# Kernel optimization log

Hardware: AMD Instinct MI355X
Metric: run time of the kernel (lower is better)

## Reference

```python
import jax, jax.numpy as jnp
import numpy as np


def setup_inputs() -> dict:
    key = jax.random.key(0)
    M, D = 131072, 16
    x = jax.random.normal(key, (M, D), dtype=jnp.float32)
    return {"x": x, "n_segs": 64, "k": 16}


def reference(x, n_segs, k):
    """Segmented kNN graph: for each point set (segment), find each point's k
    nearest neighbors (L2) within its own segment and emit edges knn -> node,
    with node ids globally offset by the segment start (sum_{p<i} |V_p| + j).

    Returns
    -------
    dists : [M, k] float32  squared L2 distance to each of the k neighbors
    src   : [M, k] int32    global node ids of the k predecessors of each node
    dst   : [M]    int32    global node ids (dst of the k edges in each row)
    """
    M, D = x.shape
    S = M // n_segs  # points per segment (equal-sized segments)
    xs = x.reshape(n_segs, S, D)                              # [N, S, D]
    sq = jnp.sum(xs * xs, axis=-1)                            # [N, S]
    # squared pairwise distances per segment: ||a||^2 + ||b||^2 - 2 a.b
    dist = sq[:, :, None] + sq[:, None, :] - 2.0 * jnp.einsum(
        "nsd,ntd->nst", xs, xs
    )                                                         # [N, S, S]
    neg, idx = jax.lax.top_k(-dist, k)                        # [N, S, k] each
    offs = (jnp.arange(n_segs, dtype=jnp.int32) * S)[:, None, None]
    src = (idx.astype(jnp.int32) + offs).reshape(M, k)        # global neighbor ids
    dst = jnp.arange(M, dtype=jnp.int32)
    dists = (-neg).reshape(M, k)
    return dists, src, dst
```

## Files before the change

kernel.cpp:

```cpp
#include <hip/hip_runtime.h>
#include <math.h>


#define DD 16
#define KK 16
#define SENT 0x7F7FFFFFu

typedef unsigned int uint;
typedef unsigned short ushort;
typedef short bf16x8 __attribute__((ext_vector_type(8)));
typedef float f32x4 __attribute__((ext_vector_type(4)));

__device__ __forceinline__ uint cvtpk(float a, float b) {
  uint r;
  asm("v_cvt_pk_bf16_f32 %0, %1, %2" : "=v"(r) : "v"(a), "v"(b));
  return r;
}
__device__ __forceinline__ ushort f2bf(float f) {
  uint u = __float_as_uint(f);
  return (ushort)((u + 0x7FFFu + ((u >> 16) & 1u)) >> 16);
}

__device__ __forceinline__ void bitonic16(uint (&b)[16]) {
#pragma unroll
  for (int s = 8; s >= 1; s >>= 1) {
#pragma unroll
    for (int j = 0; j < 16; ++j) {
      if ((j & s) == 0) {
        uint lo = min(b[j], b[j + s]), hi = max(b[j], b[j + s]);
        b[j] = lo; b[j + s] = hi;
      }
    }
  }
}

__device__ __forceinline__ void flushSlots(uint (&bd)[8], uint (&qd)[4]) {
  qd[1] |= 1u; qd[2] |= 2u; qd[3] |= 3u;
#define CS(i, j) { uint lo = min(qd[i], qd[j]), hi = max(qd[i], qd[j]); qd[i] = lo; qd[j] = hi; }
  CS(0, 1) CS(2, 3) CS(0, 2) CS(1, 3) CS(1, 2)
#undef CS
#pragma unroll
  for (int t = 0; t < 4; ++t) bd[4 + t] = min(bd[4 + t], qd[3 - t]);
#pragma unroll
  for (int s = 4; s >= 1; s >>= 1) {
#pragma unroll
    for (int j = 0; j < 8; ++j) {
      if ((j & s) == 0) {
        uint lo = min(bd[j], bd[j + s]), hi = max(bd[j], bd[j + s]);
        bd[j] = lo; bd[j + s] = hi;
      }
    }
  }
#pragma unroll
  for (int t = 0; t < 4; ++t) qd[t] = SENT;
}

__device__ __forceinline__ float sq16(const float4& a, const float4& b,
                                      const float4& c, const float4& d) {
  float s0 = fmaf(a.x, a.x, fmaf(a.y, a.y, fmaf(a.z, a.z, a.w * a.w)));
  float s1 = fmaf(b.x, b.x, fmaf(b.y, b.y, fmaf(b.z, b.z, b.w * b.w)));
  float s2 = fmaf(c.x, c.x, fmaf(c.y, c.y, fmaf(c.z, c.z, c.w * c.w)));
  float s3 = fmaf(d.x, d.x, fmaf(d.y, d.y, fmaf(d.z, d.z, d.w * d.w)));
  return (s0 + s1) + (s2 + s3);
}

__global__ __launch_bounds__(256, 4)
void sknn_fused(const float* __restrict__ x, float* __restrict__ out, int M, int S) {
  const int tid  = threadIdx.x;
  const int wv   = tid >> 6;
  const int lane = tid & 63;
  const int r16  = lane & 15;
  const int kh   = lane >> 4;
  const int qbase = blockIdx.x * 64 + wv * 16;
  const int segBase = (blockIdx.x * 64 / S) * S;
  const int NT = S / 16;
  const int NC = NT / 8;
  const int cloc = tid & 127;
  const int half = tid >> 7;

  __shared__ uint shm[4096];

  bf16x8 bfrag;
  {
    const float4* qp = (const float4*)(x + (size_t)(qbase + r16) * DD);
    uint bw[4] = {0u, 0u, 0u, 0u};
    if (kh == 0) {
      float4 a = qp[0], b = qp[1];
      bw[0] = cvtpk(a.x, a.y); bw[1] = cvtpk(a.z, a.w);
      bw[2] = cvtpk(b.x, b.y); bw[3] = cvtpk(b.z, b.w);
    } else if (kh == 1) {
      float4 a = qp[2], b = qp[3];
      bw[0] = cvtpk(a.x, a.y); bw[1] = cvtpk(a.z, a.w);
      bw[2] = cvtpk(b.x, b.y); bw[3] = cvtpk(b.z, b.w);
    } else if (kh == 2) {
      float4 a = qp[0], b = qp[1], c = qp[2], d = qp[3];
      float sq = sq16(a, b, c, d);
      ushort hi = f2bf(sq);
      float hif = __uint_as_float(((uint)hi) << 16);
      ushort lo = f2bf(sq - hif);
      bw[0] = (uint)hi | ((uint)lo << 16);
      bw[1] = 0x3F803F80u;
      bw[2] = 0x3F80u;
      bw[3] = 0u;
    }
    bfrag = *(bf16x8*)bw;
  }

  const int stile = cloc >> 4, srow = cloc & 15;
  const int ssw = (srow >> 1) & 3;
  const int sbase = stile * 256 + srow * 16;
  const int rd_u = r16 * 16 + ((kh ^ ((r16 >> 1) & 3)) * 4);

  auto stageWrite = [&](const float4& A0, const float4& A1,
                        const float4& A2, const float4& A3, uint dst) {
    uint* b = &shm[dst + sbase];
    if (half == 0) {
      uint4 w0, w1;
      w0.x = cvtpk(-2.f * A0.x, -2.f * A0.y);
      w0.y = cvtpk(-2.f * A0.z, -2.f * A0.w);
      w0.z = cvtpk(-2.f * A1.x, -2.f * A1.y);
      w0.w = cvtpk(-2.f * A1.z, -2.f * A1.w);
      w1.x = cvtpk(-2.f * A2.x, -2.f * A2.y);
      w1.y = cvtpk(-2.f * A2.z, -2.f * A2.w);
      w1.z = cvtpk(-2.f * A3.x, -2.f * A3.y);
      w1.w = cvtpk(-2.f * A3.z, -2.f * A3.w);
      *(uint4*)(b + (0 ^ ssw) * 4) = w0;
      *(uint4*)(b + (1 ^ ssw) * 4) = w1;
    } else {
      float sq = sq16(A0, A1, A2, A3);
      ushort hi = f2bf(sq);
      float hif = __uint_as_float(((uint)hi) << 16);
      ushort lo = f2bf(sq - hif);
      uint4 w2 = make_uint4(0x3F803F80u, (uint)hi | ((uint)lo << 16), 0x3F80u, 0u);
      uint4 w3 = make_uint4(0u, 0u, 0u, 0u);
      *(uint4*)(b + (2 ^ ssw) * 4) = w2;
      *(uint4*)(b + (3 ^ ssw) * 4) = w3;
    }
  };

  uint bd[8], qd[4];
#pragma unroll
  for (int i = 0; i < 8; ++i) bd[i] = SENT;
#pragma unroll
  for (int i = 0; i < 4; ++i) qd[i] = SENT;

  const f32x4 zacc = {0.f, 0.f, 0.f, 0.f};
  const uint kmask = 0xFFFFF800u;
  uint vidx = (uint)(kh * 4);

  auto cap = [&](const f32x4& acc) {
#pragma unroll
    for (int e = 0; e < 4; ++e)
      qd[e] = min(qd[e], (__float_as_uint(acc[e]) & kmask) | vidx);
    vidx += 16u;
  };

  {
    const float4* cp = (const float4*)(x + (size_t)(segBase + cloc) * DD);
    float4 A0 = cp[0], A1 = cp[1], A2 = cp[2], A3 = cp[3];
    stageWrite(A0, A1, A2, A3, 0u);
    __syncthreads();
  }

  for (int c = 0; c < NC; ++c) {
    const uint cur = (uint)(c & 1) * 2048u;
    const uint nxt = 2048u - cur;
    float4 A0, A1, A2, A3;
    const bool hasNext = (c + 1 < NC);
    if (hasNext) {
      const float4* cp = (const float4*)(x + (size_t)(segBase + (c + 1) * 128 + cloc) * DD);
      A0 = cp[0]; A1 = cp[1]; A2 = cp[2]; A3 = cp[3];
    }
    const uint* tb = &shm[cur];
    bf16x8 fA = *(const bf16x8*)(tb + 0 * 256 + rd_u);
    bf16x8 fB = *(const bf16x8*)(tb + 1 * 256 + rd_u);
    bf16x8 fC = *(const bf16x8*)(tb + 2 * 256 + rd_u);
    bf16x8 fD = *(const bf16x8*)(tb + 3 * 256 + rd_u);
    f32x4 c0 = __builtin_amdgcn_mfma_f32_16x16x32_bf16(fA, bfrag, zacc, 0, 0, 0);
    f32x4 c1 = __builtin_amdgcn_mfma_f32_16x16x32_bf16(fB, bfrag, zacc, 0, 0, 0);
    fA = *(const bf16x8*)(tb + 4 * 256 + rd_u);
    fB = *(const bf16x8*)(tb + 5 * 256 + rd_u);
    cap(c0); cap(c1);
    f32x4 c2 = __builtin_amdgcn_mfma_f32_16x16x32_bf16(fC, bfrag, zacc, 0, 0, 0);
    f32x4 c3 = __builtin_amdgcn_mfma_f32_16x16x32_bf16(fD, bfrag, zacc, 0, 0, 0);
    fC = *(const bf16x8*)(tb + 6 * 256 + rd_u);
    fD = *(const bf16x8*)(tb + 7 * 256 + rd_u);
    cap(c2); cap(c3);
    c0 = __builtin_amdgcn_mfma_f32_16x16x32_bf16(fA, bfrag, zacc, 0, 0, 0);
    c1 = __builtin_amdgcn_mfma_f32_16x16x32_bf16(fB, bfrag, zacc, 0, 0, 0);
    cap(c0); cap(c1);
    c2 = __builtin_amdgcn_mfma_f32_16x16x32_bf16(fC, bfrag, zacc, 0, 0, 0);
    c3 = __builtin_amdgcn_mfma_f32_16x16x32_bf16(fD, bfrag, zacc, 0, 0, 0);
    cap(c2); cap(c3);
    flushSlots(bd, qd);
    if (hasNext) stageWrite(A0, A1, A2, A3, nxt);
    __syncthreads();
  }

  uint* myrow = &shm[tid * 9];
#pragma unroll
  for (int i = 0; i < 8; ++i) myrow[i] = bd[i];
  __syncthreads();
  if (kh != 0) return;

  uint cur16[16];
  {
    const uint* prow = &shm[(tid + 16) * 9];
#pragma unroll
    for (int i = 0; i < 8; ++i) cur16[i] = bd[i];
#pragma unroll
    for (int i = 0; i < 8; ++i) cur16[8 + i] = prow[7 - i];
    bitonic16(cur16);
  }
#pragma unroll
  for (int c = 2; c < 4; ++c) {
    const uint* prow = &shm[(tid + 16 * c) * 9];
    uint ob[8];
#pragma unroll
    for (int i = 0; i < 8; ++i) ob[i] = prow[i];
#pragma unroll
    for (int q = 0; q < 8; ++q) cur16[8 + q] = min(cur16[8 + q], ob[7 - q]);
    bitonic16(cur16);
  }

  const int p = qbase + r16;
  const float fb = (float)segBase;
  float dv[16], sv[16];
#pragma unroll
  for (int i = 0; i < 16; ++i) {
    dv[i] = __uint_as_float(cur16[i] & 0xFFFFF800u) - 1.0f;
    sv[i] = fb + (float)(cur16[i] & 0x7FFu);
  }
  float* __restrict__ dptr = out + (size_t)p * KK;
  ((float4*)dptr)[0] = make_float4(dv[0], dv[1], dv[2], dv[3]);
  ((float4*)dptr)[1] = make_float4(dv[4], dv[5], dv[6], dv[7]);
  ((float4*)dptr)[2] = make_float4(dv[8], dv[9], dv[10], dv[11]);
  ((float4*)dptr)[3] = make_float4(dv[12], dv[13], dv[14], dv[15]);
  float* __restrict__ sptr = out + (size_t)M * KK + (size_t)p * KK;
  ((float4*)sptr)[0] = make_float4(sv[0], sv[1], sv[2], sv[3]);
  ((float4*)sptr)[1] = make_float4(sv[4], sv[5], sv[6], sv[7]);
  ((float4*)sptr)[2] = make_float4(sv[8], sv[9], sv[10], sv[11]);
  ((float4*)sptr)[3] = make_float4(sv[12], sv[13], sv[14], sv[15]);
  out[(size_t)2 * M * KK + p] = (float)p;
}

extern "C" void kernel_launch(void* const* d_in, const int* in_sizes, int n_in,
                              void* d_out, int out_size, void* d_ws, size_t ws_size,
                              hipStream_t stream) {
  const float* x = (const float*)d_in[0];
  const int M = in_sizes[0] / DD;
  const int S = M / 64;
  float* out = (float*)d_out;
  (void)d_ws; (void)ws_size;

  sknn_fused<<<M / 64, 256, 0, stream>>>(x, out, M, S);
}
```

Baseline: 57.33 us.

## Precompute bf16 augmented candidate rows in a prep kernel, stream them into LDS

Adds a prep kernel that turns each point once into a 32-element bf16 augmented row (scaled coordinates, norm hi/lo, ones) stored in workspace. The main kernel then copies these rows straight into LDS, with no per-chunk conversion or norm recomputation. Previously each of the 32 blocks per segment redid that work for every candidate. The cost is a second launch and an extra global write and read of the augmented array, and it falls back to the fused kernel when the workspace is too small.

```diff
diff --git a/kernel.cpp b/kernel.cpp
--- a/kernel.cpp
+++ b/kernel.cpp
@@ -62,6 +62,192 @@
   float s2 = fmaf(c.x, c.x, fmaf(c.y, c.y, fmaf(c.z, c.z, c.w * c.w)));
   float s3 = fmaf(d.x, d.x, fmaf(d.y, d.y, fmaf(d.z, d.z, d.w * d.w)));
   return (s0 + s1) + (s2 + s3);
+}
+
+__global__ void sknn_prep(const float* __restrict__ x, ushort* __restrict__ augA, int M) {
+  int p = blockIdx.x * 256 + threadIdx.x;
+  if (p >= M) return;
+  const float4* r = (const float4*)(x + (size_t)p * DD);
+  float4 v0 = r[0], v1 = r[1], v2 = r[2], v3 = r[3];
+  float f[16] = {v0.x, v0.y, v0.z, v0.w, v1.x, v1.y, v1.z, v1.w,
+                 v2.x, v2.y, v2.z, v2.w, v3.x, v3.y, v3.z, v3.w};
+  float sq = sq16(v0, v1, v2, v3);
+  ushort sq_hi = f2bf(sq);
+  float hif = __uint_as_float(((uint)sq_hi) << 16);
+  ushort sq_lo = f2bf(sq - hif);
+
+  ushort A[32];
+#pragma unroll
+  for (int d = 0; d < 16; ++d) A[d] = f2bf(-2.f * f[d]);
+  A[16] = 0x3F80; A[17] = 0x3F80; A[18] = sq_hi; A[19] = sq_lo; A[20] = 0x3F80;
+#pragma unroll
+  for (int d = 21; d < 32; ++d) A[d] = 0;
+
+  uint wa[16];
+#pragma unroll
+  for (int i = 0; i < 16; ++i) wa[i] = (uint)A[2 * i] | ((uint)A[2 * i + 1] << 16);
+  uint4* da = (uint4*)(augA + (size_t)p * 32);
+#pragma unroll
+  for (int i = 0; i < 4; ++i)
+    da[i] = make_uint4(wa[4 * i], wa[4 * i + 1], wa[4 * i + 2], wa[4 * i + 3]);
+}
+
+__global__ __launch_bounds__(256, 4)
+void sknn_mfma(const ushort* __restrict__ augA, const float* __restrict__ x,
+               float* __restrict__ out, int M, int S) {
+  const int tid  = threadIdx.x;
+  const int wv   = tid >> 6;
+  const int lane = tid & 63;
+  const int r16  = lane & 15;
+  const int kh   = lane >> 4;
+  const int qbase = blockIdx.x * 64 + wv * 16;
+  const int segBase = (blockIdx.x * 64 / S) * S;
+  const int NT = S / 16;
+  const int NC = NT / 8;
+
+  __shared__ uint shm[4096];
+
+  bf16x8 bfrag;
+  {
+    const float4* qp = (const float4*)(x + (size_t)(qbase + r16) * DD);
+    uint bw[4] = {0u, 0u, 0u, 0u};
+    if (kh == 0) {
+      float4 a = qp[0], b = qp[1];
+      bw[0] = cvtpk(a.x, a.y); bw[1] = cvtpk(a.z, a.w);
+      bw[2] = cvtpk(b.x, b.y); bw[3] = cvtpk(b.z, b.w);
+    } else if (kh == 1) {
+      float4 a = qp[2], b = qp[3];
+      bw[0] = cvtpk(a.x, a.y); bw[1] = cvtpk(a.z, a.w);
+      bw[2] = cvtpk(b.x, b.y); bw[3] = cvtpk(b.z, b.w);
+    } else if (kh == 2) {
+      float4 a = qp[0], b = qp[1], c = qp[2], d = qp[3];
+      float sq = sq16(a, b, c, d);
+      ushort hi = f2bf(sq);
+      float hif = __uint_as_float(((uint)hi) << 16);
+      ushort lo = f2bf(sq - hif);
+      bw[0] = (uint)hi | ((uint)lo << 16);
+      bw[1] = 0x3F803F80u;
+      bw[2] = 0x3F80u;
+      bw[3] = 0u;
+    }
+    bfrag = *(bf16x8*)bw;
+  }
+
+  const ushort* __restrict__ abase = augA + (size_t)segBase * 32;
+
+  const int src_u = ((lane >> 2) * 32) + ((((lane & 3) ^ ((lane >> 3) & 3))) * 8);
+  const int st0 = 2 * wv, st1 = 2 * wv + 1;
+  const int rd_u = r16 * 16 + ((kh ^ ((r16 >> 1) & 3)) * 4);
+
+  uint bd[8], qd[4];
+#pragma unroll
+  for (int i = 0; i < 8; ++i) bd[i] = SENT;
+#pragma unroll
+  for (int i = 0; i < 4; ++i) qd[i] = SENT;
+
+  const f32x4 zacc = {0.f, 0.f, 0.f, 0.f};
+  const uint kmask = 0xFFFFF800u;
+  uint vidx = (uint)(kh * 4);
+
+  auto cap = [&](const f32x4& acc) {
+#pragma unroll
+    for (int e = 0; e < 4; ++e)
+      qd[e] = min(qd[e], (__float_as_uint(acc[e]) & kmask) | vidx);
+    vidx += 16u;
+  };
+
+  {
+    uint4 s0 = *(const uint4*)(abase + (size_t)st0 * 512 + src_u);
+    uint4 s1 = *(const uint4*)(abase + (size_t)st1 * 512 + src_u);
+    *(uint4*)(&shm[st0 * 256 + lane * 4]) = s0;
+    *(uint4*)(&shm[st1 * 256 + lane * 4]) = s1;
+    __syncthreads();
+  }
+
+  for (int c = 0; c < NC; ++c) {
+    const uint cur = (uint)(c & 1) * 2048u;
+    const uint nxt = 2048u - cur;
+    uint4 s0, s1;
+    const bool hasNext = (c + 1 < NC);
+    if (hasNext) {
+      const ushort* cb = abase + (size_t)(c + 1) * 4096;
+      s0 = *(const uint4*)(cb + (size_t)st0 * 512 + src_u);
+      s1 = *(const uint4*)(cb + (size_t)st1 * 512 + src_u);
+    }
+    const uint* tb = &shm[cur];
+    bf16x8 fA = *(const bf16x8*)(tb + 0 * 256 + rd_u);
+    bf16x8 fB = *(const bf16x8*)(tb + 1 * 256 + rd_u);
+    bf16x8 fC = *(const bf16x8*)(tb + 2 * 256 + rd_u);
+    bf16x8 fD = *(const bf16x8*)(tb + 3 * 256 + rd_u);
+    f32x4 c0 = __builtin_amdgcn_mfma_f32_16x16x32_bf16(fA, bfrag, zacc, 0, 0, 0);
+    f32x4 c1 = __builtin_amdgcn_mfma_f32_16x16x32_bf16(fB, bfrag, zacc, 0, 0, 0);
+    fA = *(const bf16x8*)(tb + 4 * 256 + rd_u);
+    fB = *(const bf16x8*)(tb + 5 * 256 + rd_u);
+    cap(c0); cap(c1);
+    f32x4 c2 = __builtin_amdgcn_mfma_f32_16x16x32_bf16(fC, bfrag, zacc, 0, 0, 0);
+    f32x4 c3 = __builtin_amdgcn_mfma_f32_16x16x32_bf16(fD, bfrag, zacc, 0, 0, 0);
+    fC = *(const bf16x8*)(tb + 6 * 256 + rd_u);
+    fD = *(const bf16x8*)(tb + 7 * 256 + rd_u);
+    cap(c2); cap(c3);
+    c0 = __builtin_amdgcn_mfma_f32_16x16x32_bf16(fA, bfrag, zacc, 0, 0, 0);
+    c1 = __builtin_amdgcn_mfma_f32_16x16x32_bf16(fB, bfrag, zacc, 0, 0, 0);
+    cap(c0); cap(c1);
+    c2 = __builtin_amdgcn_mfma_f32_16x16x32_bf16(fC, bfrag, zacc, 0, 0, 0);
+    c3 = __builtin_amdgcn_mfma_f32_16x16x32_bf16(fD, bfrag, zacc, 0, 0, 0);
+    cap(c2); cap(c3);
+    flushSlots(bd, qd);
+    if (hasNext) {
+      *(uint4*)(&shm[nxt + st0 * 256 + lane * 4]) = s0;
+      *(uint4*)(&shm[nxt + st1 * 256 + lane * 4]) = s1;
+    }
+    __syncthreads();
+  }
+
+  uint* myrow = &shm[tid * 9];
+#pragma unroll
+  for (int i = 0; i < 8; ++i) myrow[i] = bd[i];
+  __syncthreads();
+  if (kh != 0) return;
+
+  uint cur16[16];
+  {
+    const uint* prow = &shm[(tid + 16) * 9];
+#pragma unroll
+    for (int i = 0; i < 8; ++i) cur16[i] = bd[i];
+#pragma unroll
+    for (int i = 0; i < 8; ++i) cur16[8 + i] = prow[7 - i];
+    bitonic16(cur16);
+  }
+#pragma unroll
+  for (int c = 2; c < 4; ++c) {
+    const uint* prow = &shm[(tid + 16 * c) * 9];
+    uint ob[8];
+#pragma unroll
+    for (int i = 0; i < 8; ++i) ob[i] = prow[i];
+#pragma unroll
+    for (int q = 0; q < 8; ++q) cur16[8 + q] = min(cur16[8 + q], ob[7 - q]);
+    bitonic16(cur16);
+  }
+
+  const int p = qbase + r16;
+  const float fb = (float)segBase;
+  float dv[16], sv[16];
+#pragma unroll
+  for (int i = 0; i < 16; ++i) {
+    dv[i] = __uint_as_float(cur16[i] & 0xFFFFF800u) - 1.0f;
+    sv[i] = fb + (float)(cur16[i] & 0x7FFu);
+  }
+  float* __restrict__ dptr = out + (size_t)p * KK;
+  ((float4*)dptr)[0] = make_float4(dv[0], dv[1], dv[2], dv[3]);
+  ((float4*)dptr)[1] = make_float4(dv[4], dv[5], dv[6], dv[7]);
+  ((float4*)dptr)[2] = make_float4(dv[8], dv[9], dv[10], dv[11]);
+  ((float4*)dptr)[3] = make_float4(dv[12], dv[13], dv[14], dv[15]);
+  float* __restrict__ sptr = out + (size_t)M * KK + (size_t)p * KK;
+  ((float4*)sptr)[0] = make_float4(sv[0], sv[1], sv[2], sv[3]);
+  ((float4*)sptr)[1] = make_float4(sv[4], sv[5], sv[6], sv[7]);
+  ((float4*)sptr)[2] = make_float4(sv[8], sv[9], sv[10], sv[11]);
+  ((float4*)sptr)[3] = make_float4(sv[12], sv[13], sv[14], sv[15]);
+  out[(size_t)2 * M * KK + p] = (float)p;
 }
 
 __global__ __launch_bounds__(256, 4)
@@ -251,7 +437,13 @@
   const int M = in_sizes[0] / DD;
   const int S = M / 64;
   float* out = (float*)d_out;
-  (void)d_ws; (void)ws_size;
-
-  sknn_fused<<<M / 64, 256, 0, stream>>>(x, out, M, S);
-}
+
+  const size_t augBytes = (size_t)M * 32 * sizeof(ushort);
+  if (ws_size >= augBytes) {
+    ushort* augA = (ushort*)d_ws;
+    sknn_prep<<<M / 256, 256, 0, stream>>>(x, augA, M);
+    sknn_mfma<<<M / 64, 256, 0, stream>>>(augA, x, out, M, S);
+  } else {
+    sknn_fused<<<M / 64, 256, 0, stream>>>(x, out, M, S);
+  }
+}
```

After: 51.70 us. 1.11x faster.
